# Optimization experiments

Hardware: AMD Instinct MI355X
Metric: run time of the kernel (lower is better)

## Reference

```python
import jax, jax.numpy as jnp
import numpy as np
from jax import lax

B, C, H, W = 4, 64, 96, 320
RC = C // 4                     # reduced channels = 16
D = 48                          # max_disp = len(norm_disp_range)
NORM_DISP = jnp.arange(D, dtype=jnp.float32) / 160.0
EPS = 1e-5


def conv2d(x, w, b=None, pad=0, groups=1):
    y = lax.conv_general_dilated(x, w, (1, 1), ((pad, pad), (pad, pad)),
                                 dimension_numbers=('NCHW', 'OIHW', 'NCHW'),
                                 feature_group_count=groups)
    if b is not None:
        y = y + b[None, :, None, None]
    return y


def group_norm(x, g, b, groups=8):
    n, c, h, w = x.shape
    xg = x.reshape(n, groups, c // groups, h, w)
    mu = xg.mean(axis=(2, 3, 4), keepdims=True)
    var = xg.var(axis=(2, 3, 4), keepdims=True)
    xn = ((xg - mu) * lax.rsqrt(var + EPS)).reshape(n, c, h, w)
    return xn * g[None, :, None, None] + b[None, :, None, None]


elu = jax.nn.elu


def setup_inputs() -> dict:
    key = jax.random.key(0)
    ks = iter(jax.random.split(key, 32))

    def rn(shape, scale=0.05):
        return jax.random.normal(next(ks), shape, dtype=jnp.float32) * scale

    inp = {
        'left_feat': jax.random.normal(next(ks), (B, C, H, W), jnp.float32),
        'right_feat': jax.random.normal(next(ks), (B, C, H, W), jnp.float32),
        'directs': jnp.ones((B,), jnp.float32),
        # q_conv / k_conv: 1x1 conv (no bias) + GroupNorm(8) params
        'qw': rn((RC, C, 1, 1)), 'q_g': jnp.ones((RC,)), 'q_b': jnp.zeros((RC,)),
        'kw': rn((RC, C, 1, 1)), 'k_g': jnp.ones((RC,)), 'k_b': jnp.zeros((RC,)),
        # global_attn: avgpool -> 1x1 (rc->rc/2) -> ELU -> 1x1 (rc/2->rc)
        'ga_w1': rn((RC // 2, RC, 1, 1)), 'ga_b1': jnp.zeros((RC // 2,)),
        'ga_w2': rn((RC, RC // 2, 1, 1)), 'ga_b2': jnp.zeros((RC,)),
        # local_attn: 3x3 conv + GN(8) + ELU
        'la_w': rn((RC, RC, 3, 3)), 'la_b': jnp.zeros((RC,)),
        'la_g': jnp.ones((RC,)), 'la_bb': jnp.zeros((RC,)),
        # attn_fusion: 1x1 (2rc->rc) -> ELU -> 1x1 (rc->D)
        'af_w1': rn((RC, 2 * RC, 1, 1)), 'af_b1': jnp.zeros((RC,)),
        'af_w2': rn((D, RC, 1, 1)), 'af_b2': jnp.zeros((D,)),
        # refine_cost: depthwise 3x3 (groups=D) -> ELU -> 1x1
        'rdw_w': rn((D, 1, 3, 3)), 'rdw_b': jnp.zeros((D,)),
        'rpw_w': rn((D, D, 1, 1)), 'rpw_b': jnp.zeros((D,)),
        # fusion: reflection-pad 3x3 conv (C+D -> C) + SELayer(C, 16)
        'fu_w': rn((C, C + D, 3, 3)), 'fu_b': jnp.zeros((C,)),
        'se_w1': rn((C // 16, C)), 'se_w2': rn((C, C // 16)),
    }
    return inp


def reference(left_feat, right_feat, directs, qw, q_g, q_b, kw, k_g, k_b,
              ga_w1, ga_b1, ga_w2, ga_b2, la_w, la_b, la_g, la_bb,
              af_w1, af_b1, af_w2, af_b2, rdw_w, rdw_b, rpw_w, rpw_b,
              fu_w, fu_b, se_w1, se_w2):
    q = elu(group_norm(conv2d(left_feat, qw), q_g, q_b))      # [B,RC,H,W]
    k = elu(group_norm(conv2d(right_feat, kw), k_g, k_b))     # [B,RC,H,W]

    gp = q.mean(axis=(2, 3), keepdims=True)                   # AdaptiveAvgPool2d(1)
    gfeat = conv2d(elu(conv2d(gp, ga_w1, ga_b1)), ga_w2, ga_b2)
    gfeat = jnp.broadcast_to(gfeat, q.shape)
    lfeat = elu(group_norm(conv2d(q, la_w, la_b, pad=1), la_g, la_bb))
    comb = jnp.concatenate([gfeat, lfeat], axis=1)            # [B,2RC,H,W]
    attn = conv2d(elu(conv2d(comb, af_w1, af_b1)), af_w2, af_b2)  # [B,D,H,W]

    # Warped cost volume. grid_sample shifts only the x-coordinate by
    # disp*2*directs (normalized, align_corners=True), i.e. a constant
    # horizontal shift of disp*directs*(W-1) pixels with border clamping.
    # Channel-mean commutes with horizontal bilinear sampling, so warp
    # the channel-mean map directly (identical math, D x less work).
    km = k.mean(axis=1)                                       # [B,H,W]
    shift = NORM_DISP[None, :] * directs[:, None] * (W - 1)   # [B,D]
    pos = jnp.arange(W, dtype=jnp.float32)[None, None, :] + shift[:, :, None]  # [B,D,W]
    x0 = jnp.floor(pos)
    f = pos - x0                                              # bilinear frac
    i0 = jnp.clip(x0, 0, W - 1).astype(jnp.int32)
    i1 = jnp.clip(x0 + 1, 0, W - 1).astype(jnp.int32)

    def gather(idx):  # km[b,h,idx[b,d,w]] -> [B,D,H,W]
        return jnp.take_along_axis(
            km[:, None, :, :],
            jnp.broadcast_to(idx[:, :, None, :], (B, D, H, W)), axis=3)

    fw = f[:, :, None, :]
    warped = gather(i0) * (1.0 - fw) + gather(i1) * fw        # [B,D,H,W]
    vol = warped * jax.nn.sigmoid(attn)                       # sigmoid-weighted volume

    cost = conv2d(elu(conv2d(vol, rdw_w, rdw_b, pad=1, groups=D)), rpw_w, rpw_b)
    norm_cost = jax.nn.softmax(cost, axis=1)

    # fusion: ReflectionPad2d(1) + 3x3 conv, SE layer, ELU
    cat = jnp.concatenate([left_feat, norm_cost], axis=1)     # [B,C+D,H,W]
    cat_p = jnp.pad(cat, ((0, 0), (0, 0), (1, 1), (1, 1)), mode='reflect')
    fused = conv2d(cat_p, fu_w, fu_b)                         # [B,C,H,W]
    y = fused.mean(axis=(2, 3))                               # [B,C]
    y = jax.nn.sigmoid(jax.nn.relu(y @ se_w1.T) @ se_w2.T)
    x = elu(fused * y[:, :, None, None])
    return (x, norm_cost)
```

## Files before the change

### kernel.cpp

```cpp
#include <hip/hip_runtime.h>
#include <math.h>

static constexpr int B_  = 4;
static constexpr int C_  = 64;
static constexpr int H_  = 96;
static constexpr int W_  = 320;
static constexpr int HW  = H_ * W_;
static constexpr int RCH = 16;
static constexpr int D_  = 48;
static constexpr int NG  = 8;
static constexpr int CPG = RCH / NG;
static constexpr float EPS_ = 1e-5f;
static constexpr int APX = 322;

typedef __attribute__((ext_vector_type(8))) short short8;
typedef __attribute__((ext_vector_type(4))) float f32x4;
typedef __attribute__((ext_vector_type(4))) unsigned int u32x4;

__device__ __forceinline__ float elu1(float x) { return x > 0.f ? x : __expf(x) - 1.f; }
__device__ __forceinline__ float sigm(float x) { return 1.f / (1.f + __expf(-x)); }
__device__ __forceinline__ unsigned bf16rne(float f) {
    unsigned u = __builtin_bit_cast(unsigned, f);
    u += 0x7fffu + ((u >> 16) & 1u);
    return u >> 16;
}
__device__ __forceinline__ void gload16(const void* g, void* l) {
    __builtin_amdgcn_global_load_lds((const __attribute__((address_space(1))) unsigned int*)g,
                                     (__attribute__((address_space(3))) unsigned int*)l, 16, 0, 0);
}

__global__ __launch_bounds__(256) void k_wrepack(
    const float* __restrict__ qw, const float* __restrict__ kw, const float* __restrict__ law,
    float* __restrict__ qwp, float* __restrict__ kwp, float* __restrict__ lawp)
{
    int t = threadIdx.x;
    for (int i = t; i < RCH * C_; i += 256) {
        int c = i >> 4, r = i & 15;
        qwp[i] = qw[r * C_ + c];
        kwp[i] = kw[r * C_ + c];
    }
    for (int i = t; i < RCH * RCH * 9; i += 256) {
        int co = i & 15, rest = i >> 4;
        int ci = rest / 9, tap = rest % 9;
        lawp[i] = law[(co * RCH + ci) * 9 + tap];
    }
}

__global__ __launch_bounds__(256) void k_conv_qk(
    const float* __restrict__ left, const float* __restrict__ right,
    const float* __restrict__ qwp, const float* __restrict__ kwp,
    float* __restrict__ qraw, float* __restrict__ kraw)
{
    int idx = blockIdx.x * 256 + threadIdx.x;
    int half = idx / (B_ * HW / 2);
    int r0 = idx - half * (B_ * HW / 2);
    int b = r0 / (HW / 2), p2 = r0 - b * (HW / 2);
    int p = p2 * 2;
    const float* src = (half ? right : left) + (size_t)b * C_ * HW + p;
    const float* wp  = half ? kwp : qwp;
    float* dst = (half ? kraw : qraw) + (size_t)b * RCH * HW + p;
    float2 acc[RCH];
#pragma unroll
    for (int r = 0; r < RCH; r++) acc[r] = make_float2(0.f, 0.f);
#pragma unroll
    for (int c = 0; c < C_; c++) {
        float2 v = *reinterpret_cast<const float2*>(src + (size_t)c * HW);
        const float* wrow = wp + c * RCH;
#pragma unroll
        for (int r = 0; r < RCH; r++) {
            acc[r].x += v.x * wrow[r];
            acc[r].y += v.y * wrow[r];
        }
    }
#pragma unroll
    for (int r = 0; r < RCH; r++)
        *reinterpret_cast<float2*>(dst + (size_t)r * HW) = acc[r];
}

__global__ __launch_bounds__(256) void k_gn_stats(const float* __restrict__ src, float* __restrict__ stats)
{
    int b = blockIdx.x / NG, g = blockIdx.x % NG;
    const float4* base = (const float4*)(src + ((size_t)b * RCH + g * CPG) * HW);
    float s = 0.f, ss = 0.f;
    for (int i = threadIdx.x; i < CPG * HW / 4; i += 256) {
        float4 v = base[i];
        s  += v.x + v.y + v.z + v.w;
        ss += v.x * v.x + v.y * v.y + v.z * v.z + v.w * v.w;
    }
    __shared__ float rs[256], rq[256];
    rs[threadIdx.x] = s; rq[threadIdx.x] = ss; __syncthreads();
    for (int off = 128; off > 0; off >>= 1) {
        if (threadIdx.x < off) { rs[threadIdx.x] += rs[threadIdx.x + off]; rq[threadIdx.x] += rq[threadIdx.x + off]; }
        __syncthreads();
    }
    if (threadIdx.x == 0) {
        float inv = 1.f / (float)(CPG * HW);
        float m = rs[0] * inv;
        float var = rq[0] * inv - m * m;
        stats[blockIdx.x * 2 + 0] = m;
        stats[blockIdx.x * 2 + 1] = rsqrtf(var + EPS_);
    }
}

__global__ __launch_bounds__(256) void k_gn_apply(float* __restrict__ x, const float* __restrict__ stats,
    const float* __restrict__ gam, const float* __restrict__ bet)
{
    int idx4 = blockIdx.x * 256 + threadIdx.x;
    int b = idx4 / (RCH * HW / 4);
    int rc = (idx4 / (HW / 4)) % RCH;
    int g = rc >> 1;
    float m = stats[(b * NG + g) * 2], is = stats[(b * NG + g) * 2 + 1];
    float ga = gam[rc] * is, be = bet[rc] - m * is * gam[rc];
    float4 v = ((const float4*)x)[idx4];
    v.x = elu1(v.x * ga + be); v.y = elu1(v.y * ga + be);
    v.z = elu1(v.z * ga + be); v.w = elu1(v.w * ga + be);
    ((float4*)x)[idx4] = v;
}

__global__ __launch_bounds__(256) void k_km(const float* __restrict__ kraw, const float* __restrict__ stats,
    const float* __restrict__ gam, const float* __restrict__ bet, float* __restrict__ km)
{
    int idx = blockIdx.x * 256 + threadIdx.x;
    int b = idx / HW, p = idx - b * HW;
    float s = 0.f;
#pragma unroll
    for (int rc = 0; rc < RCH; rc++) {
        int g = rc >> 1;
        float m = stats[(b * NG + g) * 2], is = stats[(b * NG + g) * 2 + 1];
        float v = (kraw[((size_t)b * RCH + rc) * HW + p] - m) * is * gam[rc] + bet[rc];
        s += elu1(v);
    }
    km[idx] = s * (1.f / (float)RCH);
}

__global__ __launch_bounds__(256) void k_rowmean(const float* __restrict__ src, float* __restrict__ out)
{
    const float4* base = (const float4*)(src + (size_t)blockIdx.x * HW);
    float s = 0.f;
    for (int p = threadIdx.x; p < HW / 4; p += 256) {
        float4 v = base[p];
        s += v.x + v.y + v.z + v.w;
    }
    __shared__ float red[256];
    red[threadIdx.x] = s; __syncthreads();
    for (int off = 128; off > 0; off >>= 1) {
        if (threadIdx.x < off) red[threadIdx.x] += red[threadIdx.x + off];
        __syncthreads();
    }
    if (threadIdx.x == 0) out[blockIdx.x] = red[0] * (1.f / (float)HW);
}

__global__ __launch_bounds__(64) void k_gfeat(const float* __restrict__ gp,
    const float* __restrict__ gaw1, const float* __restrict__ gab1,
    const float* __restrict__ gaw2, const float* __restrict__ gab2,
    const float* __restrict__ afw1, const float* __restrict__ afb1,
    float* __restrict__ gbias)
{
    __shared__ float g1[B_ * 8], gf[B_ * RCH];
    int t = threadIdx.x;
    if (t < B_ * 8) {
        int b = t >> 3, o = t & 7;
        float a = gab1[o];
        for (int i = 0; i < RCH; i++) a += gaw1[o * RCH + i] * gp[b * RCH + i];
        g1[b * 8 + o] = elu1(a);
    }
    __syncthreads();
    {
        int b = t >> 4, o = t & 15;
        float a = gab2[o];
        for (int i = 0; i < 8; i++) a += gaw2[o * 8 + i] * g1[b * 8 + i];
        gf[t] = a;
    }
    __syncthreads();
    {
        int b = t >> 4, o = t & 15;
        float a = afb1[o];
        for (int i = 0; i < RCH; i++) a += afw1[o * 2 * RCH + i] * gf[b * RCH + i];
        gbias[t] = a;
    }
}

__global__ __launch_bounds__(256) void k_conv_la(const float* __restrict__ q,
    const float* __restrict__ lawp, const float* __restrict__ lab, float* __restrict__ lraw)
{
    int idx = blockIdx.x * 256 + threadIdx.x;
    int b = idx / HW, p = idx - b * HW;
    int h = p / W_, w = p - h * W_;
    float acc[RCH];
#pragma unroll
    for (int co = 0; co < RCH; co++) acc[co] = lab[co];
#pragma unroll
    for (int ci = 0; ci < RCH; ci++) {
        const float* qb = q + ((size_t)b * RCH + ci) * HW;
#pragma unroll
        for (int kh = 0; kh < 3; kh++) {
            int hh = h + kh - 1;
            if (hh < 0 || hh >= H_) continue;
            float a0 = (w - 1 >= 0) ? qb[hh * W_ + w - 1] : 0.f;
            float a1 = qb[hh * W_ + w];
            float a2 = (w + 1 < W_) ? qb[hh * W_ + w + 1] : 0.f;
            const float* wp0 = lawp + (ci * 9 + kh * 3) * RCH;
#pragma unroll
            for (int co = 0; co < RCH; co++)
                acc[co] += a0 * wp0[co] + a1 * wp0[RCH + co] + a2 * wp0[2 * RCH + co];
        }
    }
#pragma unroll
    for (int co = 0; co < RCH; co++) lraw[((size_t)b * RCH + co) * HW + p] = acc[co];
}

__global__ __launch_bounds__(256) void k_vol(const float* __restrict__ lraw,
    const float* __restrict__ stats, const float* __restrict__ lg, const float* __restrict__ lb,
    const float* __restrict__ gbias, const float* __restrict__ afw1,
    const float* __restrict__ afw2, const float* __restrict__ afb2,
    const float* __restrict__ km, const float* __restrict__ directs, float* __restrict__ vol)
{
    __shared__ float w1[RCH * 2 * RCH];
    __shared__ float w2[D_ * RCH];
    __shared__ float b2[D_];
    for (int i = threadIdx.x; i < RCH * 2 * RCH; i += 256) w1[i] = afw1[i];
    for (int i = threadIdx.x; i < D_ * RCH; i += 256) w2[i] = afw2[i];
    if (threadIdx.x < D_) b2[threadIdx.x] = afb2[threadIdx.x];
    __syncthreads();
    int idx = blockIdx.x * 256 + threadIdx.x;
    int b = idx / HW, p = idx - b * HW;
    int h = p / W_, w = p - h * W_;
    float lf[RCH];
#pragma unroll
    for (int rc = 0; rc < RCH; rc++) {
        int g = rc >> 1;
        float m = stats[(b * NG + g) * 2], is = stats[(b * NG + g) * 2 + 1];
        lf[rc] = elu1((lraw[((size_t)b * RCH + rc) * HW + p] - m) * is * lg[rc] + lb[rc]);
    }
    float hid[RCH];
#pragma unroll
    for (int o = 0; o < RCH; o++) {
        float a = gbias[b * RCH + o];
#pragma unroll
        for (int i = 0; i < RCH; i++) a += w1[o * 2 * RCH + RCH + i] * lf[i];
        hid[o] = elu1(a);
    }
    const float* kmrow = km + (size_t)b * HW + h * W_;
    float dir = directs[b];
    for (int d = 0; d < D_; d++) {
        float a = b2[d];
#pragma unroll
        for (int o = 0; o < RCH; o++) a += w2[d * RCH + o] * hid[o];
        float s = sigm(a);
        float shift = ((float)d / 160.f) * dir * (float)(W_ - 1);
        float pos = (float)w + shift;
        float x0 = floorf(pos);
        float f = pos - x0;
        float c0 = fminf(fmaxf(x0, 0.f), (float)(W_ - 1));
        float c1 = fminf(fmaxf(x0 + 1.f, 0.f), (float)(W_ - 1));
        int i0 = (int)c0, i1 = (int)c1;
        float wv = kmrow[i0] * (1.f - f) + kmrow[i1] * f;
        vol[((size_t)(b * D_ + d)) * HW + p] = wv * s;
    }
}

__global__ __launch_bounds__(256) void k_dw(const float* __restrict__ vol,
    const float* __restrict__ wgt, const float* __restrict__ bias, float* __restrict__ dwout)
{
    int idx = blockIdx.x * 256 + threadIdx.x;
    int p4 = idx % (HW / 4);
    int d  = (idx / (HW / 4)) % D_;
    int b  = idx / (D_ * HW / 4);
    int h = p4 / (W_ / 4), w = (p4 % (W_ / 4)) * 4;
    const float* vb = vol + ((size_t)(b * D_ + d)) * HW;
    float wz[9];
#pragma unroll
    for (int i = 0; i < 9; i++) wz[i] = wgt[d * 9 + i];
    float bv = bias[d];
    float acc[4] = {bv, bv, bv, bv};
#pragma unroll
    for (int r = 0; r < 3; r++) {
        int hh = h + r - 1;
        if (hh < 0 || hh >= H_) continue;
        const float* row = vb + hh * W_;
        float4 c = *(const float4*)(row + w);
        float in6[6];
        in6[0] = (w > 0) ? row[w - 1] : 0.f;
        in6[1] = c.x; in6[2] = c.y; in6[3] = c.z; in6[4] = c.w;
        in6[5] = (w + 4 < W_) ? row[w + 4] : 0.f;
#pragma unroll
        for (int j = 0; j < 4; j++)
            acc[j] += in6[j] * wz[r * 3] + in6[j + 1] * wz[r * 3 + 1] + in6[j + 2] * wz[r * 3 + 2];
    }
    float4 o;
    o.x = elu1(acc[0]); o.y = elu1(acc[1]); o.z = elu1(acc[2]); o.w = elu1(acc[3]);
    ((float4*)dwout)[idx] = o;
}

__global__ __launch_bounds__(256) void k_prep(const float* __restrict__ left, unsigned int* __restrict__ abf)
{
    int idx = blockIdx.x * 256 + threadIdx.x;
    int px = idx % APX;
    int bh = idx / APX;
    int b = bh / H_, h = bh % H_;
    int w = px - 1;
    w = w < 0 ? -w : (w >= W_ ? 2 * W_ - 2 - w : w);
    const float* src = left + (size_t)b * C_ * HW + h * W_ + w;
    unsigned int* dst = abf + (size_t)idx * 60;
#pragma unroll
    for (int q4 = 0; q4 < 8; q4++) {
        u32x4 t;
#pragma unroll
        for (int z = 0; z < 4; z++) {
            int ci = (q4 * 4 + z) * 2;
            float f0 = src[(size_t)ci * HW];
            float f1 = src[(size_t)(ci + 1) * HW];
            t[z] = bf16rne(f0) | (bf16rne(f1) << 16);
        }
        *reinterpret_cast<u32x4*>(dst + q4 * 4) = t;
    }
    *reinterpret_cast<u32x4*>(dst + 56) = (u32x4){0u, 0u, 0u, 0u};
}

__global__ __launch_bounds__(256) void k_rpw(const float* __restrict__ dwin,
    const float* __restrict__ wgt, const float* __restrict__ bias,
    float* __restrict__ ncost, unsigned int* __restrict__ abf)
{
    __shared__ float wr[D_ * D_];
    __shared__ float bs[D_];
    for (int i = threadIdx.x; i < D_ * D_; i += 256) wr[i] = wgt[i];
    if (threadIdx.x < D_) bs[threadIdx.x] = bias[threadIdx.x];
    __syncthreads();
    int idx = blockIdx.x * 256 + threadIdx.x;
    int b = idx / HW, p = idx - b * HW;
    int h = p / W_, w = p - h * W_;
    float v[D_];
#pragma unroll
    for (int i = 0; i < D_; i++) v[i] = dwin[((size_t)(b * D_ + i)) * HW + p];
    float cst[D_];
    float mx = -1e30f;
#pragma unroll
    for (int d = 0; d < D_; d++) {
        float a = bs[d];
        const float4* wrow = (const float4*)&wr[d * D_];
#pragma unroll
        for (int i4 = 0; i4 < D_ / 4; i4++) {
            float4 wv = wrow[i4];
            a += wv.x * v[i4 * 4 + 0] + wv.y * v[i4 * 4 + 1]
               + wv.z * v[i4 * 4 + 2] + wv.w * v[i4 * 4 + 3];
        }
        cst[d] = a; mx = fmaxf(mx, a);
    }
    float s = 0.f;
#pragma unroll
    for (int d = 0; d < D_; d++) { float e = __expf(cst[d] - mx); cst[d] = e; s += e; }
    float inv = 1.f / s;
#pragma unroll
    for (int d = 0; d < D_; d++) {
        cst[d] *= inv;
        ncost[((size_t)(b * D_ + d)) * HW + p] = cst[d];
    }
    u32x4 pk[6];
#pragma unroll
    for (int q4 = 0; q4 < 6; q4++)
#pragma unroll
        for (int z = 0; z < 4; z++) {
            int d = (q4 * 4 + z) * 2;
            pk[q4][z] = bf16rne(cst[d]) | (bf16rne(cst[d + 1]) << 16);
        }
    size_t bh322 = (size_t)(b * H_ + h) * APX;
    unsigned int* dst = abf + (bh322 + (w + 1)) * 60 + 32;
#pragma unroll
    for (int q4 = 0; q4 < 6; q4++) *reinterpret_cast<u32x4*>(dst + q4 * 4) = pk[q4];
    if (w == 1 || w == W_ - 2) {
        unsigned int* dst2 = abf + (bh322 + (w == 1 ? 0 : APX - 1)) * 60 + 32;
#pragma unroll
        for (int q4 = 0; q4 < 6; q4++) *reinterpret_cast<u32x4*>(dst2 + q4 * 4) = pk[q4];
    }
}

__global__ __launch_bounds__(256) void k_wpack(const float* __restrict__ fw, unsigned short* __restrict__ wpack)
{
    int bi = blockIdx.x;
    int tap = bi >> 2, kblk = bi & 3;
    int kh = tap / 3, kw2 = tap % 3;
    int t = threadIdx.x;
    int ct = t >> 6, l = t & 63;
    int co = ct * 16 + (l & 15);
    int ci0 = kblk * 32 + ((l >> 4) & 3) * 8;
    unsigned short v[8];
#pragma unroll
    for (int j = 0; j < 8; j++) {
        int ci = ci0 + j;
        float f = (ci < 112) ? fw[((size_t)(co * 112 + ci)) * 9 + kh * 3 + kw2] : 0.f;
        v[j] = (unsigned short)bf16rne(f);
    }
    *reinterpret_cast<short8*>(wpack + ((size_t)bi * 256 + t) * 8) = *reinterpret_cast<short8*>(v);
}

static constexpr int LROWB  = 240;
static constexpr int LPLANB = 66 * LROWB;
__global__ __launch_bounds__(256, 1) void k_fused_mfma(
    const unsigned int* __restrict__ abf,
    const unsigned short* __restrict__ wpack, const float* __restrict__ fb,
    float* __restrict__ fused)
{
    __shared__ __align__(16) unsigned int Atile4[15844];
    int bb = blockIdx.z;
    int h0 = blockIdx.y * 2;
    int w0 = blockIdx.x * 64;
    int tid = threadIdx.x;
    int wid = tid >> 6;
    int l   = tid & 63;

    {
        int hh = h0 - 1 + wid;
        hh = hh < 0 ? -hh : (hh >= H_ ? 2 * H_ - 2 - hh : hh);
        const char* gsrc = (const char*)(abf + ((size_t)(bb * H_ + hh) * APX + w0) * 60);
        char* lbase = (char*)Atile4 + wid * LPLANB;
#pragma unroll
        for (int i = 0; i < 15; i++)
            gload16(gsrc + (i * 64 + l) * 16, lbase + i * 1024);
        if (l < 30) gload16(gsrc + (960 + l) * 16, lbase + 15 * 1024);
    }
    __syncthreads();

    int row = wid >> 1;
    int ch  = wid & 1;
    int li = l & 15, lg = l >> 4;

    const short8* __restrict__ wp8 = reinterpret_cast<const short8*>(wpack);

    f32x4 acc[4][2];
    float bv0 = fb[(ch * 2 + 0) * 16 + li];
    float bv1 = fb[(ch * 2 + 1) * 16 + li];
#pragma unroll
    for (int pt = 0; pt < 4; pt++) {
        acc[pt][0] = (f32x4){bv0, bv0, bv0, bv0};
        acc[pt][1] = (f32x4){bv1, bv1, bv1, bv1};
    }

    const char* Abase = (const char*)Atile4;
#pragma unroll
    for (int kh = 0; kh < 3; kh++) {
#pragma unroll
        for (int kw2 = 0; kw2 < 3; kw2++) {
#pragma unroll
            for (int kblk = 0; kblk < 4; kblk++) {
                int step = (kh * 3 + kw2) * 4 + kblk;
                short8 b0 = wp8[step * 256 + (ch * 2 + 0) * 64 + l];
                short8 b1 = wp8[step * 256 + (ch * 2 + 1) * 64 + l];
                int rbase = (row + kh) * LPLANB + kblk * 64 + lg * 16 + (kw2 + li) * LROWB;
#pragma unroll
                for (int pt = 0; pt < 4; pt++) {
                    short8 a = *reinterpret_cast<const short8*>(Abase + rbase + pt * (16 * LROWB));
                    acc[pt][0] = __builtin_amdgcn_mfma_f32_16x16x32_bf16(a, b0, acc[pt][0], 0, 0, 0);
                    acc[pt][1] = __builtin_amdgcn_mfma_f32_16x16x32_bf16(a, b1, acc[pt][1], 0, 0, 0);
                }
            }
        }
    }

    int h = h0 + row;
#pragma unroll
    for (int j = 0; j < 2; j++) {
        int co = (ch * 2 + j) * 16 + li;
        float* ob = fused + ((size_t)(bb * C_ + co) * H_ + h) * W_ + w0 + lg * 4;
#pragma unroll
        for (int pt = 0; pt < 4; pt++) {
            *reinterpret_cast<f32x4*>(ob + pt * 16) = acc[pt][j];
        }
    }
}

__global__ __launch_bounds__(256) void k_se(const float* __restrict__ ymean,
    const float* __restrict__ w1, const float* __restrict__ w2, float* __restrict__ scale)
{
    __shared__ float h4[B_ * 4];
    int t = threadIdx.x;
    if (t < B_ * 4) {
        int b = t >> 2, o = t & 3;
        float a = 0.f;
        for (int c = 0; c < C_; c++) a += w1[o * C_ + c] * ymean[b * C_ + c];
        h4[b * 4 + o] = fmaxf(a, 0.f);
    }
    __syncthreads();
    {
        int b = t >> 6, c = t & 63;
        float a = 0.f;
        for (int o = 0; o < 4; o++) a += w2[c * 4 + o] * h4[b * 4 + o];
        scale[t] = sigm(a);
    }
}

__global__ __launch_bounds__(256) void k_final(const float* __restrict__ fused,
    const float* __restrict__ scale, float* __restrict__ out)
{
    int idx4 = blockIdx.x * 256 + threadIdx.x;
    int bc = idx4 / (HW / 4);
    float sc = scale[bc];
    float4 v = ((const float4*)fused)[idx4];
    v.x = elu1(v.x * sc); v.y = elu1(v.y * sc);
    v.z = elu1(v.z * sc); v.w = elu1(v.w * sc);
    ((float4*)out)[idx4] = v;
}

extern "C" void kernel_launch(void* const* d_in, const int* in_sizes, int n_in,
                              void* d_out, int out_size, void* d_ws, size_t ws_size,
                              hipStream_t stream)
{
    const float* left   = (const float*)d_in[0];
    const float* right  = (const float*)d_in[1];
    const float* directs= (const float*)d_in[2];
    const float* qw     = (const float*)d_in[3];
    const float* q_g    = (const float*)d_in[4];
    const float* q_b    = (const float*)d_in[5];
    const float* kw     = (const float*)d_in[6];
    const float* k_g    = (const float*)d_in[7];
    const float* k_b    = (const float*)d_in[8];
    const float* gaw1   = (const float*)d_in[9];
    const float* gab1   = (const float*)d_in[10];
    const float* gaw2   = (const float*)d_in[11];
    const float* gab2   = (const float*)d_in[12];
    const float* law    = (const float*)d_in[13];
    const float* lab    = (const float*)d_in[14];
    const float* lag    = (const float*)d_in[15];
    const float* labb   = (const float*)d_in[16];
    const float* afw1   = (const float*)d_in[17];
    const float* afb1   = (const float*)d_in[18];
    const float* afw2   = (const float*)d_in[19];
    const float* afb2   = (const float*)d_in[20];
    const float* rdww   = (const float*)d_in[21];
    const float* rdwb   = (const float*)d_in[22];
    const float* rpww   = (const float*)d_in[23];
    const float* rpwb   = (const float*)d_in[24];
    const float* fuw    = (const float*)d_in[25];
    const float* fub    = (const float*)d_in[26];
    const float* sew1   = (const float*)d_in[27];
    const float* sew2   = (const float*)d_in[28];

    float* ws    = (float*)d_ws;
    float* qraw  = ws + 0;
    float* kraw  = ws + 1966080;
    float* km    = ws + 3932160;
    float* vol   = ws + 4055040;
    float* dwb   = ws + 9953280;
    float* smal  = ws + 15851520;
    unsigned int* abf = (unsigned int*)(ws + 0);
    float* fused = ws + 7418880;
    float* lraw  = kraw;
    unsigned short* wpack = (unsigned short*)(ws + 15811584);

    float* qwp   = dwb + 0;
    float* kwp   = dwb + 1024;
    float* lawp  = dwb + 2048;

    float* stQ   = smal + 0;
    float* stK   = smal + 64;
    float* stL   = smal + 128;
    float* gp    = smal + 192;
    float* gbias = smal + 256;
    float* ymean = smal + 320;
    float* scal  = smal + 576;

    float* xout  = (float*)d_out;
    float* ncost = xout + 7864320;

    k_wrepack<<<1, 256, 0, stream>>>(qw, kw, law, qwp, kwp, lawp);
    k_conv_qk<<<480, 256, 0, stream>>>(left, right, qwp, kwp, qraw, kraw);
    k_gn_stats<<<32, 256, 0, stream>>>(qraw, stQ);
    k_gn_stats<<<32, 256, 0, stream>>>(kraw, stK);
    k_gn_apply<<<1920, 256, 0, stream>>>(qraw, stQ, q_g, q_b);
    k_km<<<480, 256, 0, stream>>>(kraw, stK, k_g, k_b, km);
    k_rowmean<<<64, 256, 0, stream>>>(qraw, gp);
    k_gfeat<<<1, 64, 0, stream>>>(gp, gaw1, gab1, gaw2, gab2, afw1, afb1, gbias);
    k_conv_la<<<480, 256, 0, stream>>>(qraw, lawp, lab, lraw);
    k_gn_stats<<<32, 256, 0, stream>>>(lraw, stL);
    k_vol<<<480, 256, 0, stream>>>(lraw, stL, lag, labb, gbias, afw1, afw2, afb2, km, directs, vol);
    k_dw<<<5760, 256, 0, stream>>>(vol, rdww, rdwb, dwb);
    k_prep<<<483, 256, 0, stream>>>(left, abf);
    k_rpw<<<480, 256, 0, stream>>>(dwb, rpww, rpwb, ncost, abf);
    k_wpack<<<36, 256, 0, stream>>>(fuw, wpack);
    k_fused_mfma<<<dim3(5, 48, 4), 256, 0, stream>>>(abf, wpack, fub, fused);
    k_rowmean<<<256, 256, 0, stream>>>(fused, ymean);
    k_se<<<1, 256, 0, stream>>>(ymean, sew1, sew2, scal);
    k_final<<<7680, 256, 0, stream>>>(fused, scal, xout);
}
```

Measured before the change: 272.5 us.

## Fuse depthwise conv into pointwise kernel and fold reductions into producers

Removes the separate depthwise-conv kernel by recomputing the 3x3 depthwise conv inside the pointwise/softmax kernel. This eliminates a full write and read of a 48-channel intermediate volume. The two row-mean kernels are replaced by wave-reduced atomic adds inside the GN-apply and MFMA conv kernels. The Q/K GroupNorm stats launches are merged into one. k_vol now maps one block per image row and stages the key-mean row in LDS for the gather. The costs are redundant 9-tap loads in the fused kernel and atomic contention plus non-deterministic float summation order.

```diff
diff --git a/kernel.cpp b/kernel.cpp
--- a/kernel.cpp
+++ b/kernel.cpp
@@ -31,9 +31,11 @@
 
 __global__ __launch_bounds__(256) void k_wrepack(
     const float* __restrict__ qw, const float* __restrict__ kw, const float* __restrict__ law,
-    float* __restrict__ qwp, float* __restrict__ kwp, float* __restrict__ lawp)
+    float* __restrict__ qwp, float* __restrict__ kwp, float* __restrict__ lawp,
+    float* __restrict__ gp)
 {
     int t = threadIdx.x;
+    if (t < B_ * RCH) gp[t] = 0.f;
     for (int i = t; i < RCH * C_; i += 256) {
         int c = i >> 4, r = i & 15;
         qwp[i] = qw[r * C_ + c];
@@ -77,6 +79,35 @@
         *reinterpret_cast<float2*>(dst + (size_t)r * HW) = acc[r];
 }
 
+__global__ __launch_bounds__(256) void k_gn_stats2(const float* __restrict__ qsrc,
+    const float* __restrict__ ksrc, float* __restrict__ stats)
+{
+    int z = blockIdx.x;
+    const float* src = (z < 32) ? qsrc : ksrc;
+    int zz = (z < 32) ? z : z - 32;
+    int b = zz / NG, g = zz % NG;
+    const float4* base = (const float4*)(src + ((size_t)b * RCH + g * CPG) * HW);
+    float s = 0.f, ss = 0.f;
+    for (int i = threadIdx.x; i < CPG * HW / 4; i += 256) {
+        float4 v = base[i];
+        s  += v.x + v.y + v.z + v.w;
+        ss += v.x * v.x + v.y * v.y + v.z * v.z + v.w * v.w;
+    }
+    __shared__ float rs[256], rq[256];
+    rs[threadIdx.x] = s; rq[threadIdx.x] = ss; __syncthreads();
+    for (int off = 128; off > 0; off >>= 1) {
+        if (threadIdx.x < off) { rs[threadIdx.x] += rs[threadIdx.x + off]; rq[threadIdx.x] += rq[threadIdx.x + off]; }
+        __syncthreads();
+    }
+    if (threadIdx.x == 0) {
+        float inv = 1.f / (float)(CPG * HW);
+        float m = rs[0] * inv;
+        float var = rq[0] * inv - m * m;
+        stats[z * 2 + 0] = m;
+        stats[z * 2 + 1] = rsqrtf(var + EPS_);
+    }
+}
+
 __global__ __launch_bounds__(256) void k_gn_stats(const float* __restrict__ src, float* __restrict__ stats)
 {
     int b = blockIdx.x / NG, g = blockIdx.x % NG;
@@ -103,7 +134,7 @@
 }
 
 __global__ __launch_bounds__(256) void k_gn_apply(float* __restrict__ x, const float* __restrict__ stats,
-    const float* __restrict__ gam, const float* __restrict__ bet)
+    const float* __restrict__ gam, const float* __restrict__ bet, float* __restrict__ gp)
 {
     int idx4 = blockIdx.x * 256 + threadIdx.x;
     int b = idx4 / (RCH * HW / 4);
@@ -115,6 +146,10 @@
     v.x = elu1(v.x * ga + be); v.y = elu1(v.y * ga + be);
     v.z = elu1(v.z * ga + be); v.w = elu1(v.w * ga + be);
     ((float4*)x)[idx4] = v;
+    float s = v.x + v.y + v.z + v.w;
+    s += __shfl_xor(s, 1);  s += __shfl_xor(s, 2);  s += __shfl_xor(s, 4);
+    s += __shfl_xor(s, 8);  s += __shfl_xor(s, 16); s += __shfl_xor(s, 32);
+    if ((threadIdx.x & 63) == 0) atomicAdd(&gp[b * RCH + rc], s);
 }
 
 __global__ __launch_bounds__(256) void k_km(const float* __restrict__ kraw, const float* __restrict__ stats,
@@ -133,23 +168,6 @@
     km[idx] = s * (1.f / (float)RCH);
 }
 
-__global__ __launch_bounds__(256) void k_rowmean(const float* __restrict__ src, float* __restrict__ out)
-{
-    const float4* base = (const float4*)(src + (size_t)blockIdx.x * HW);
-    float s = 0.f;
-    for (int p = threadIdx.x; p < HW / 4; p += 256) {
-        float4 v = base[p];
-        s += v.x + v.y + v.z + v.w;
-    }
-    __shared__ float red[256];
-    red[threadIdx.x] = s; __syncthreads();
-    for (int off = 128; off > 0; off >>= 1) {
-        if (threadIdx.x < off) red[threadIdx.x] += red[threadIdx.x + off];
-        __syncthreads();
-    }
-    if (threadIdx.x == 0) out[blockIdx.x] = red[0] * (1.f / (float)HW);
-}
-
 __global__ __launch_bounds__(64) void k_gfeat(const float* __restrict__ gp,
     const float* __restrict__ gaw1, const float* __restrict__ gab1,
     const float* __restrict__ gaw2, const float* __restrict__ gab2,
@@ -158,10 +176,11 @@
 {
     __shared__ float g1[B_ * 8], gf[B_ * RCH];
     int t = threadIdx.x;
+    const float invHW = 1.f / (float)HW;
     if (t < B_ * 8) {
         int b = t >> 3, o = t & 7;
         float a = gab1[o];
-        for (int i = 0; i < RCH; i++) a += gaw1[o * RCH + i] * gp[b * RCH + i];
+        for (int i = 0; i < RCH; i++) a += gaw1[o * RCH + i] * (gp[b * RCH + i] * invHW);
         g1[b * 8 + o] = elu1(a);
     }
     __syncthreads();
@@ -209,7 +228,7 @@
     for (int co = 0; co < RCH; co++) lraw[((size_t)b * RCH + co) * HW + p] = acc[co];
 }
 
-__global__ __launch_bounds__(256) void k_vol(const float* __restrict__ lraw,
+__global__ __launch_bounds__(320) void k_vol(const float* __restrict__ lraw,
     const float* __restrict__ stats, const float* __restrict__ lg, const float* __restrict__ lb,
     const float* __restrict__ gbias, const float* __restrict__ afw1,
     const float* __restrict__ afw2, const float* __restrict__ afb2,
@@ -218,13 +237,16 @@
     __shared__ float w1[RCH * 2 * RCH];
     __shared__ float w2[D_ * RCH];
     __shared__ float b2[D_];
-    for (int i = threadIdx.x; i < RCH * 2 * RCH; i += 256) w1[i] = afw1[i];
-    for (int i = threadIdx.x; i < D_ * RCH; i += 256) w2[i] = afw2[i];
-    if (threadIdx.x < D_) b2[threadIdx.x] = afb2[threadIdx.x];
+    __shared__ float kms[W_];
+    int blk = blockIdx.x;
+    int b = blk / H_, h = blk - b * H_;
+    int t = threadIdx.x;
+    for (int i = t; i < RCH * 2 * RCH; i += 320) w1[i] = afw1[i];
+    for (int i = t; i < D_ * RCH; i += 320) w2[i] = afw2[i];
+    if (t < D_) b2[t] = afb2[t];
+    kms[t] = km[(size_t)b * HW + h * W_ + t];
     __syncthreads();
-    int idx = blockIdx.x * 256 + threadIdx.x;
-    int b = idx / HW, p = idx - b * HW;
-    int h = p / W_, w = p - h * W_;
+    int w = t, p = h * W_ + w;
     float lf[RCH];
 #pragma unroll
     for (int rc = 0; rc < RCH; rc++) {
@@ -240,7 +262,6 @@
         for (int i = 0; i < RCH; i++) a += w1[o * 2 * RCH + RCH + i] * lf[i];
         hid[o] = elu1(a);
     }
-    const float* kmrow = km + (size_t)b * HW + h * W_;
     float dir = directs[b];
     for (int d = 0; d < D_; d++) {
         float a = b2[d];
@@ -254,42 +275,9 @@
         float c0 = fminf(fmaxf(x0, 0.f), (float)(W_ - 1));
         float c1 = fminf(fmaxf(x0 + 1.f, 0.f), (float)(W_ - 1));
         int i0 = (int)c0, i1 = (int)c1;
-        float wv = kmrow[i0] * (1.f - f) + kmrow[i1] * f;
+        float wv = kms[i0] * (1.f - f) + kms[i1] * f;
         vol[((size_t)(b * D_ + d)) * HW + p] = wv * s;
     }
-}
-
-__global__ __launch_bounds__(256) void k_dw(const float* __restrict__ vol,
-    const float* __restrict__ wgt, const float* __restrict__ bias, float* __restrict__ dwout)
-{
-    int idx = blockIdx.x * 256 + threadIdx.x;
-    int p4 = idx % (HW / 4);
-    int d  = (idx / (HW / 4)) % D_;
-    int b  = idx / (D_ * HW / 4);
-    int h = p4 / (W_ / 4), w = (p4 % (W_ / 4)) * 4;
-    const float* vb = vol + ((size_t)(b * D_ + d)) * HW;
-    float wz[9];
-#pragma unroll
-    for (int i = 0; i < 9; i++) wz[i] = wgt[d * 9 + i];
-    float bv = bias[d];
-    float acc[4] = {bv, bv, bv, bv};
-#pragma unroll
-    for (int r = 0; r < 3; r++) {
-        int hh = h + r - 1;
-        if (hh < 0 || hh >= H_) continue;
-        const float* row = vb + hh * W_;
-        float4 c = *(const float4*)(row + w);
-        float in6[6];
-        in6[0] = (w > 0) ? row[w - 1] : 0.f;
-        in6[1] = c.x; in6[2] = c.y; in6[3] = c.z; in6[4] = c.w;
-        in6[5] = (w + 4 < W_) ? row[w + 4] : 0.f;
-#pragma unroll
-        for (int j = 0; j < 4; j++)
-            acc[j] += in6[j] * wz[r * 3] + in6[j + 1] * wz[r * 3 + 1] + in6[j + 2] * wz[r * 3 + 2];
-    }
-    float4 o;
-    o.x = elu1(acc[0]); o.y = elu1(acc[1]); o.z = elu1(acc[2]); o.w = elu1(acc[3]);
-    ((float4*)dwout)[idx] = o;
 }
 
 __global__ __launch_bounds__(256) void k_prep(const float* __restrict__ left, unsigned int* __restrict__ abf)
@@ -317,7 +305,8 @@
     *reinterpret_cast<u32x4*>(dst + 56) = (u32x4){0u, 0u, 0u, 0u};
 }
 
-__global__ __launch_bounds__(256) void k_rpw(const float* __restrict__ dwin,
+__global__ __launch_bounds__(256) void k_dwrpw(const float* __restrict__ vol,
+    const float* __restrict__ dww, const float* __restrict__ dwbias,
     const float* __restrict__ wgt, const float* __restrict__ bias,
     float* __restrict__ ncost, unsigned int* __restrict__ abf)
 {
@@ -331,7 +320,21 @@
     int h = p / W_, w = p - h * W_;
     float v[D_];
 #pragma unroll
-    for (int i = 0; i < D_; i++) v[i] = dwin[((size_t)(b * D_ + i)) * HW + p];
+    for (int d = 0; d < D_; d++) {
+        const float* vb = vol + ((size_t)(b * D_ + d)) * HW;
+        float a = dwbias[d];
+#pragma unroll
+        for (int r = 0; r < 3; r++) {
+            int hh = h + r - 1;
+            if (hh < 0 || hh >= H_) continue;
+            const float* row = vb + hh * W_;
+            float a0 = (w > 0) ? row[w - 1] : 0.f;
+            float a1 = row[w];
+            float a2 = (w + 1 < W_) ? row[w + 1] : 0.f;
+            a += a0 * dww[d * 9 + r * 3] + a1 * dww[d * 9 + r * 3 + 1] + a2 * dww[d * 9 + r * 3 + 2];
+        }
+        v[d] = elu1(a);
+    }
     float cst[D_];
     float mx = -1e30f;
 #pragma unroll
@@ -374,12 +377,14 @@
     }
 }
 
-__global__ __launch_bounds__(256) void k_wpack(const float* __restrict__ fw, unsigned short* __restrict__ wpack)
+__global__ __launch_bounds__(256) void k_wpack(const float* __restrict__ fw, unsigned short* __restrict__ wpack,
+    float* __restrict__ ymean)
 {
     int bi = blockIdx.x;
+    int t = threadIdx.x;
+    if (bi == 0 && t < B_ * C_) ymean[t] = 0.f;
     int tap = bi >> 2, kblk = bi & 3;
     int kh = tap / 3, kw2 = tap % 3;
-    int t = threadIdx.x;
     int ct = t >> 6, l = t & 63;
     int co = ct * 16 + (l & 15);
     int ci0 = kblk * 32 + ((l >> 4) & 3) * 8;
@@ -398,7 +403,7 @@
 __global__ __launch_bounds__(256, 1) void k_fused_mfma(
     const unsigned int* __restrict__ abf,
     const unsigned short* __restrict__ wpack, const float* __restrict__ fb,
-    float* __restrict__ fused)
+    float* __restrict__ fused, float* __restrict__ ymean)
 {
     __shared__ __align__(16) unsigned int Atile4[15844];
     int bb = blockIdx.z;
@@ -466,6 +471,17 @@
             *reinterpret_cast<f32x4*>(ob + pt * 16) = acc[pt][j];
         }
     }
+    float s0 = 0.f, s1 = 0.f;
+#pragma unroll
+    for (int pt = 0; pt < 4; pt++)
+#pragma unroll
+        for (int rg = 0; rg < 4; rg++) { s0 += acc[pt][0][rg]; s1 += acc[pt][1][rg]; }
+    s0 += __shfl_xor(s0, 16); s0 += __shfl_xor(s0, 32);
+    s1 += __shfl_xor(s1, 16); s1 += __shfl_xor(s1, 32);
+    if (lg == 0) {
+        atomicAdd(&ymean[bb * C_ + (ch * 2 + 0) * 16 + li], s0);
+        atomicAdd(&ymean[bb * C_ + (ch * 2 + 1) * 16 + li], s1);
+    }
 }
 
 __global__ __launch_bounds__(256) void k_se(const float* __restrict__ ymean,
@@ -473,10 +489,11 @@
 {
     __shared__ float h4[B_ * 4];
     int t = threadIdx.x;
+    const float invHW = 1.f / (float)HW;
     if (t < B_ * 4) {
         int b = t >> 2, o = t & 3;
         float a = 0.f;
-        for (int c = 0; c < C_; c++) a += w1[o * C_ + c] * ymean[b * C_ + c];
+        for (int c = 0; c < C_; c++) a += w1[o * C_ + c] * (ymean[b * C_ + c] * invHW);
         h4[b * 4 + o] = fmaxf(a, 0.f);
     }
     __syncthreads();
@@ -538,20 +555,18 @@
     float* qraw  = ws + 0;
     float* kraw  = ws + 1966080;
     float* km    = ws + 3932160;
-    float* vol   = ws + 4055040;
-    float* dwb   = ws + 9953280;
+    float* vol   = ws + 9953280;
     float* smal  = ws + 15851520;
     unsigned int* abf = (unsigned int*)(ws + 0);
     float* fused = ws + 7418880;
     float* lraw  = kraw;
     unsigned short* wpack = (unsigned short*)(ws + 15811584);
 
-    float* qwp   = dwb + 0;
-    float* kwp   = dwb + 1024;
-    float* lawp  = dwb + 2048;
+    float* qwp   = ws + 4055040;
+    float* kwp   = ws + 4056064;
+    float* lawp  = ws + 4057088;
 
     float* stQ   = smal + 0;
-    float* stK   = smal + 64;
     float* stL   = smal + 128;
     float* gp    = smal + 192;
     float* gbias = smal + 256;
@@ -561,23 +576,19 @@
     float* xout  = (float*)d_out;
     float* ncost = xout + 7864320;
 
-    k_wrepack<<<1, 256, 0, stream>>>(qw, kw, law, qwp, kwp, lawp);
+    k_wrepack<<<1, 256, 0, stream>>>(qw, kw, law, qwp, kwp, lawp, gp);
     k_conv_qk<<<480, 256, 0, stream>>>(left, right, qwp, kwp, qraw, kraw);
-    k_gn_stats<<<32, 256, 0, stream>>>(qraw, stQ);
-    k_gn_stats<<<32, 256, 0, stream>>>(kraw, stK);
-    k_gn_apply<<<1920, 256, 0, stream>>>(qraw, stQ, q_g, q_b);
-    k_km<<<480, 256, 0, stream>>>(kraw, stK, k_g, k_b, km);
-    k_rowmean<<<64, 256, 0, stream>>>(qraw, gp);
+    k_gn_stats2<<<64, 256, 0, stream>>>(qraw, kraw, stQ);
+    k_gn_apply<<<1920, 256, 0, stream>>>(qraw, stQ, q_g, q_b, gp);
+    k_km<<<480, 256, 0, stream>>>(kraw, stQ + 64, k_g, k_b, km);
     k_gfeat<<<1, 64, 0, stream>>>(gp, gaw1, gab1, gaw2, gab2, afw1, afb1, gbias);
     k_conv_la<<<480, 256, 0, stream>>>(qraw, lawp, lab, lraw);
     k_gn_stats<<<32, 256, 0, stream>>>(lraw, stL);
-    k_vol<<<480, 256, 0, stream>>>(lraw, stL, lag, labb, gbias, afw1, afw2, afb2, km, directs, vol);
-    k_dw<<<5760, 256, 0, stream>>>(vol, rdww, rdwb, dwb);
+    k_vol<<<384, 320, 0, stream>>>(lraw, stL, lag, labb, gbias, afw1, afw2, afb2, km, directs, vol);
     k_prep<<<483, 256, 0, stream>>>(left, abf);
-    k_rpw<<<480, 256, 0, stream>>>(dwb, rpww, rpwb, ncost, abf);
-    k_wpack<<<36, 256, 0, stream>>>(fuw, wpack);
-    k_fused_mfma<<<dim3(5, 48, 4), 256, 0, stream>>>(abf, wpack, fub, fused);
-    k_rowmean<<<256, 256, 0, stream>>>(fused, ymean);
+    k_dwrpw<<<480, 256, 0, stream>>>(vol, rdww, rdwb, rpww, rpwb, ncost, abf);
+    k_wpack<<<36, 256, 0, stream>>>(fuw, wpack, ymean);
+    k_fused_mfma<<<dim3(5, 48, 4), 256, 0, stream>>>(abf, wpack, fub, fused, ymean);
     k_se<<<1, 256, 0, stream>>>(ymean, sew1, sew2, scal);
     k_final<<<7680, 256, 0, stream>>>(fused, scal, xout);
 }
```

After: 333.5 us. 22.4% more time.
